# Performance work log

Hardware: AMD Instinct MI355X
Metric: run time of the kernel (lower is better)

The kernel has to match this reference:

```python
import jax, jax.numpy as jnp
import numpy as np

B, N = 2, 200
IMG = 2048
NC = 4                    # node concepts ('Is*')
NODE_CH = NC * 256        # 1024
EC = 3                    # edge concepts minus 'HigherPri'
AC = 4                    # actions
BBOX_MAX = 1024.0
E = N * (N - 1)

# static fully-connected directed edge list (src=i, dst=j, i!=j), row-major order
_ii, _jj = np.meshgrid(np.arange(N), np.arange(N), indexing='ij')
_m = _ii != _jj
SRC = jnp.asarray(_ii[_m])
DST = jnp.asarray(_jj[_m])


def _lin(k, fin, fout):
    kw, kb = jax.random.split(k)
    s = 1.0 / np.sqrt(fin)
    return (jax.random.uniform(kw, (fin, fout), jnp.float32, -s, s),
            jax.random.uniform(kb, (fout,), jnp.float32, -s, s))


def setup_inputs():
    ks = jax.random.split(jax.random.key(0), 16)
    p = {}
    p['roi_features'] = jax.random.normal(ks[0], (B, N, IMG), jnp.float32)
    p['batch_bboxes'] = jax.random.uniform(ks[1], (B, N, 4), jnp.float32) * BBOX_MAX
    p['batch_directions'] = jax.random.normal(ks[2], (B, N, 4), jnp.float32)
    p['batch_priorities'] = jax.random.normal(ks[3], (B, N), jnp.float32)
    p['w1'], p['b1'] = _lin(ks[4], IMG, 512)
    p['w2'], p['b2'] = _lin(ks[5], 512, 256)
    p['w3'], p['b3'] = _lin(ks[6], 256, NODE_CH)
    p['wi'], p['bi'] = _lin(ks[7], NODE_CH, NC)
    p['we1'], p['be1'] = _lin(ks[8], 16, 256)
    p['we2'], p['be2'] = _lin(ks[9], 256, 64)
    p['we3'], p['be3'] = _lin(ks[10], 64, EC)
    p['wp1'], p['bp1'] = _lin(ks[11], EC + 1, 128)
    p['wp2'], p['bp2'] = _lin(ks[12], 128, NODE_CH * AC)
    p['root_w'], _ = _lin(ks[13], NODE_CH, AC)
    _, p['root_b'] = _lin(ks[14], NODE_CH, AC)
    return p


def reference(roi_features, batch_bboxes, batch_directions, batch_priorities,
              w1, b1, w2, b2, w3, b3, wi, bi,
              we1, be1, we2, be2, we3, be3,
              wp1, bp1, wp2, bp2, root_w, root_b):
    # node concept embedding MLP: [B,N,IMG] -> [B,N,NODE_CH]
    h = jax.nn.relu(roi_features @ w1 + b1)
    h = jax.nn.relu(h @ w2 + b2)
    node_concepts = h @ w3 + b3
    node_concepts_explicit = jax.nn.sigmoid(node_concepts @ wi + bi)

    # pairwise attributes for all directed edges (same ordering as torch masks)
    node_attr = jnp.concatenate([batch_bboxes / BBOX_MAX, batch_directions], -1)  # [B,N,8]
    pair = jnp.concatenate([node_attr[:, SRC], node_attr[:, DST]], -1)            # [B,E,16]
    eh = jax.nn.relu(pair @ we1 + be1)
    eh = jax.nn.relu(eh @ we2 + be2)
    edge_attributes = jax.nn.sigmoid(eh @ we3 + be3)                              # [B,E,EC]
    higher_pri = (batch_priorities[:, SRC] > batch_priorities[:, DST]).astype(jnp.float32)
    edge_attributes = jnp.concatenate([edge_attributes, higher_pri[..., None]], -1)  # [B,E,EC+1]

    # NNConv on graph 0: per-edge weight matrix, gather-matmul-scatter
    x = node_concepts[0]                 # [N, NODE_CH]
    e = edge_attributes[0]               # [E, EC+1]
    w = jax.nn.relu(e @ wp1 + bp1) @ wp2 + bp2
    w = w.reshape(E, NODE_CH, AC)        # [E, NODE_CH, AC]
    msg = jnp.einsum('ei,eio->eo', x[SRC], w)          # [E, AC]
    agg = jax.ops.segment_sum(msg, DST, num_segments=N)  # [N, AC]
    next_actions = agg + x @ root_w + root_b
    return (next_actions, node_concepts_explicit[0], edge_attributes[0])
```

## Files before the change

### kernel.cpp

```cpp
#include <hip/hip_runtime.h>
#include <math.h>

#define NN 200
#define ETOT 39800

typedef float float4v __attribute__((ext_vector_type(4)));
typedef short short8 __attribute__((ext_vector_type(8)));
typedef unsigned int uint4v __attribute__((ext_vector_type(4)));

__device__ __forceinline__ float sigf(float x) { return 1.0f / (1.0f + expf(-x)); }

__device__ __forceinline__ unsigned short f2b(float f) {
  unsigned u = __float_as_uint(f);
  u += 0x7fffu + ((u >> 16) & 1u);
  return (unsigned short)(u >> 16);
}
__device__ __forceinline__ float b2f16(unsigned short u) {
  return __uint_as_float(((unsigned)u) << 16);
}
__device__ __forceinline__ unsigned pk2(float a, float b) {
  unsigned r;
  asm("v_cvt_pk_bf16_f32 %0, %1, %2" : "=v"(r) : "v"(a), "v"(b));
  return r;
}

__global__ __launch_bounds__(256) void k_prep(
    const float* __restrict__ w1, const float* __restrict__ w2, const float* __restrict__ w3,
    const float* __restrict__ b3, const float* __restrict__ wp2, const float* __restrict__ we2,
    const float* __restrict__ bbox, const float* __restrict__ dir,
    const float* __restrict__ we1, const float* __restrict__ be1,
    const float* __restrict__ roi, const float* __restrict__ wp1,
    const float* __restrict__ wi, const float* __restrict__ rootw, const float* __restrict__ bp2,
    unsigned short* __restrict__ w1T, unsigned short* __restrict__ w2T,
    unsigned short* __restrict__ Ac, unsigned short* __restrict__ Bc,
    unsigned short* __restrict__ we2T, unsigned short* __restrict__ roiB,
    float* __restrict__ P, float* __restrict__ Q, float* __restrict__ wp1T) {
  __shared__ float lds[64][65];
  const int b = blockIdx.x, tid = threadIdx.x;

  if (b < 288) {
    const float* Wf;
    unsigned short* Wt;
    int K, N, t;
    if (b < 256) { Wf = w1; Wt = w1T; K = 2048; N = 512; t = b; }
    else { Wf = w2; Wt = w2T; K = 512; N = 256; t = b - 256; }
    const int K64 = K >> 6;
    const int kt = t % K64, nt = t / K64;
#pragma unroll 4
    for (int i = 0; i < 16; ++i) {
      int idx = tid + i * 256;
      int r = idx >> 6, c = idx & 63;
      lds[r][c] = Wf[(size_t)(kt * 64 + r) * N + nt * 64 + c];
    }
    __syncthreads();
#pragma unroll 4
    for (int i = 0; i < 16; ++i) {
      int idx = tid + i * 256;
      int r = idx >> 6, c = idx & 63;
      Wt[(size_t)(nt * 64 + r) * K + kt * 64 + c] = f2b(lds[c][r]);
    }
  } else if (b < 416) {
    int k = b - 288;
    int o = tid >> 6, l = tid & 63;
    const float* src = wp2 + (size_t)k * 4096;
    unsigned short* dst = Ac + (size_t)(k * 4 + o) * 1024;
    for (int i = l; i < 1024; i += 64) dst[i] = f2b(src[i * 4 + o]);
  } else if (b < 432) {
    int r = b - 416;
    unsigned short* dst = Ac + (size_t)(512 + r) * 1024;
    const float* src = (r < 4) ? (wi + r) : (r < 8) ? (rootw + (r - 4))
                     : (r < 12) ? (bp2 + (r - 8)) : nullptr;
    for (int i = tid; i < 1024; i += 256)
      dst[i] = src ? f2b(src[i * 4]) : (unsigned short)0;
  } else if (b < 500) {
    int rb = (b - 432) * 4;
#pragma unroll
    for (int j = 0; j < 16; ++j) {
      int idx = tid + j * 256;
      int row = rb + (idx >> 10), i = idx & 1023;
      float val = (row < 256) ? w3[(size_t)row * 1024 + i] : (row == 256 ? b3[i] : 0.0f);
      Bc[(size_t)row * 1024 + i] = f2b(val);
    }
  } else if (b < 516) {
    int f = (b - 500) * 256 + tid;
    int c = f >> 6, k0 = (f & 63) * 4;
#pragma unroll
    for (int q = 0; q < 4; ++q)
      we2T[c * 256 + k0 + q] = f2b(we2[(k0 + q) * 64 + c]);
  } else if (b < 716) {
    int n = b - 516, c = tid;
    float a[8];
#pragma unroll
    for (int r = 0; r < 4; ++r) a[r] = bbox[n * 4 + r] * (1.0f / 1024.0f);
#pragma unroll
    for (int r = 0; r < 4; ++r) a[4 + r] = dir[n * 4 + r];
    float p = be1[c], q = 0.0f;
#pragma unroll
    for (int r = 0; r < 8; ++r) {
      p += a[r] * we1[r * 256 + c];
      q += a[r] * we1[(8 + r) * 256 + c];
    }
    P[n * 256 + c] = p;
    Q[n * 256 + c] = q;
  } else if (b < 916) {
    int n = b - 716;
    const float4v* R4 = (const float4v*)(roi + (size_t)n * 2048);
    unsigned long long* O = (unsigned long long*)(roiB + (size_t)n * 2048);
#pragma unroll
    for (int j = 0; j < 2; ++j) {
      int idx = tid + j * 256;
      float4v v = R4[idx];
      union { unsigned u[2]; unsigned long long ll; } pk;
      pk.u[0] = pk2(v[0], v[1]);
      pk.u[1] = pk2(v[2], v[3]);
      O[idx] = pk.ll;
    }
  } else {
    if (tid < 128) {
      float4v v = {wp1[tid], wp1[128 + tid], wp1[256 + tid], wp1[384 + tid]};
      ((float4v*)wp1T)[tid] = v;
    }
  }
}

__device__ __forceinline__ float4v mfma16(short8 a, short8 b, float4v c) {
  return __builtin_amdgcn_mfma_f32_16x16x32_bf16(a, b, c, 0, 0, 0);
}

template <int KSTEPS>
__device__ __forceinline__ float tile_core(const unsigned short* __restrict__ A,
                                           const unsigned short* __restrict__ B,
                                           int m0, int n0, int K,
                                           float (&red)[4][16][17]) {
  const int tid = threadIdx.x, lane = tid & 63, wv = tid >> 6;
  const int mr = lane & 15, quad = lane >> 4;
  const unsigned short* Ap = A + (size_t)(m0 + mr) * K + wv * (KSTEPS * 32) + quad * 8;
  const unsigned short* Bp = B + (size_t)(n0 + mr) * K + wv * (KSTEPS * 32) + quad * 8;
  float4v acc0 = {0.f, 0.f, 0.f, 0.f}, acc1 = {0.f, 0.f, 0.f, 0.f};
#pragma unroll
  for (int s = 0; s < KSTEPS; s += 2) {
    acc0 = mfma16(*(const short8*)(Ap + s * 32), *(const short8*)(Bp + s * 32), acc0);
    acc1 = mfma16(*(const short8*)(Ap + (s + 1) * 32), *(const short8*)(Bp + (s + 1) * 32), acc1);
  }
  float4v acc = acc0 + acc1;
#pragma unroll
  for (int r = 0; r < 4; ++r) red[wv][quad * 4 + r][mr] = acc[r];
  __syncthreads();
  const int row = tid >> 4, col = tid & 15;
  return red[0][row][col] + red[1][row][col] + red[2][row][col] + red[3][row][col];
}

__global__ __launch_bounds__(256) void k_gemm1_compose(
    const unsigned short* __restrict__ roiB, const unsigned short* __restrict__ w1T,
    const float* __restrict__ b1, unsigned short* __restrict__ h1,
    const unsigned short* __restrict__ Ac, const unsigned short* __restrict__ Bc,
    unsigned short* __restrict__ CT, float* __restrict__ biasT) {
  __shared__ float red[4][16][17];
  const int bid = blockIdx.x, tid = threadIdx.x;
  if (bid < 416) {
    const int m0 = (bid % 13) * 16, n0 = (bid / 13) * 16;
    float v = tile_core<16>(roiB, w1T, m0, n0, 2048, red);
    const int row = tid >> 4, col = tid & 15;
    v += b1[n0 + col];
    v = fmaxf(v, 0.f);
    h1[(size_t)(m0 + row) * 512 + n0 + col] = f2b(v);
  } else {
    const int t = bid - 416;
    const int m0 = (t % 33) * 16, n0 = (t / 33) * 16;
    float v = tile_core<8>(Ac, Bc, m0, n0, 1024, red);
    const int row = tid >> 4, col = tid & 15;
    const int c = n0 + col;
    if (c < 256) CT[(size_t)(m0 + row) * 256 + c] = f2b(v);
    else if (c == 256) biasT[m0 + row] = v;
  }
}

__global__ __launch_bounds__(256) void k_gemm2(const unsigned short* __restrict__ h1,
                                               const unsigned short* __restrict__ w2T,
                                               const float* __restrict__ b2,
                                               unsigned short* __restrict__ h2) {
  __shared__ float red[4][16][17];
  const int m0 = blockIdx.x * 16, n0 = blockIdx.y * 16, tid = threadIdx.x;
  float v = tile_core<4>(h1, w2T, m0, n0, 512, red);
  const int row = tid >> 4, col = tid & 15;
  v += b2[n0 + col];
  v = fmaxf(v, 0.f);
  h2[(size_t)(m0 + row) * 256 + n0 + col] = f2b(v);
}

__global__ __launch_bounds__(256) void k_tfused(const unsigned short* __restrict__ h2,
                                                const unsigned short* __restrict__ CT,
                                                const float* __restrict__ biasT,
                                                const float* __restrict__ bi,
                                                const float* __restrict__ rootb,
                                                float* __restrict__ Tm, float* __restrict__ out1,
                                                float* __restrict__ out0, float* __restrict__ U) {
  __shared__ float red[4][16][17];
  const int m0 = blockIdx.x * 16, n0 = blockIdx.y * 16, tid = threadIdx.x;
  float v = tile_core<2>(h2, CT, m0, n0, 256, red);
  const int row = tid >> 4, col = tid & 15;
  const int n = m0 + row, c = n0 + col;
  v += biasT[c];
  if (c < 512) {
    Tm[(size_t)n * 512 + c] = v;
  } else if (n < NN) {
    int r = c - 512;
    if (r < 4) out1[n * 4 + r] = sigf(v + bi[r]);
    else if (r < 8) out0[n * 4 + (r - 4)] = v + rootb[r - 4];
    else if (r < 12) U[n * 4 + (r - 8)] = v;
  }
}

__global__ __launch_bounds__(256) void k_edge(
    const float* __restrict__ P, const float* __restrict__ Q,
    const unsigned short* __restrict__ we2T,
    const float* __restrict__ be2, const float* __restrict__ we3, const float* __restrict__ be3,
    const float* __restrict__ wp1T, const float* __restrict__ bp1,
    const float* __restrict__ pri,
    const float* __restrict__ T, const float* __restrict__ U,
    float* __restrict__ out0, float* __restrict__ out_ea) {
  __shared__ int src_s[64], dst_s[64];
  __shared__ float ea_s[64][4];
  __shared__ float4v wp1s[128];
  __shared__ float bp1s[128];
  __shared__ float4v Ts[2][128];
  __shared__ float Us[2][4];

  const int tid = threadIdx.x;
  const int e0 = blockIdx.x * 64;
  const int s_lo = e0 / 199;

  if (tid < 64) {
    int e = e0 + tid;
    int i = -1, j = 0;
    if (e < ETOT) {
      i = e / 199;
      int jj = e - i * 199;
      j = jj + (jj >= i ? 1 : 0);
    }
    src_s[tid] = i;
    dst_s[tid] = j;
  }
  if (tid < 128) {
    wp1s[tid] = ((const float4v*)wp1T)[tid];
    bp1s[tid] = bp1[tid];
  }
  {
    int row = tid >> 7, c = tid & 127;
    Ts[row][c] = ((const float4v*)T)[(s_lo + row) * 128 + c];
  }
  if (tid < 8) {
    int s = min(s_lo + (tid >> 2), 199);
    Us[tid >> 2][tid & 3] = U[s * 4 + (tid & 3)];
  }
  __syncthreads();

  const int lane = tid & 63;
  const int wv = tid >> 6;
  const int m = lane & 15;
  const int quad = lane >> 4;
  const int eloc = wv * 16 + m;
  const int si = src_s[eloc];
  const int dj = dst_s[eloc];

  float4v acc[4];
#pragma unroll
  for (int ct = 0; ct < 4; ++ct) { acc[ct][0] = 0.f; acc[ct][1] = 0.f; acc[ct][2] = 0.f; acc[ct][3] = 0.f; }

  const short8* W8 = (const short8*)we2T;

  for (int ks = 0; ks < 8; ++ks) {
    union { short8 s; uint4v u; } af;
    af.s = (short8)0;
    if (si >= 0) {
      const float4v* p4 = (const float4v*)(P + si * 256 + ks * 32 + quad * 8);
      const float4v* q4 = (const float4v*)(Q + dj * 256 + ks * 32 + quad * 8);
      float4v v0 = p4[0] + q4[0];
      float4v v1 = p4[1] + q4[1];
      af.u[0] = pk2(fmaxf(v0[0], 0.f), fmaxf(v0[1], 0.f));
      af.u[1] = pk2(fmaxf(v0[2], 0.f), fmaxf(v0[3], 0.f));
      af.u[2] = pk2(fmaxf(v1[0], 0.f), fmaxf(v1[1], 0.f));
      af.u[3] = pk2(fmaxf(v1[2], 0.f), fmaxf(v1[3], 0.f));
    }
#pragma unroll
    for (int ct = 0; ct < 4; ++ct) {
      short8 bf = W8[(ct * 16 + m) * 32 + ks * 4 + quad];
      acc[ct] = __builtin_amdgcn_mfma_f32_16x16x32_bf16(af.s, bf, acc[ct], 0, 0, 0);
    }
  }

  float ev[4][3];
#pragma unroll
  for (int r = 0; r < 4; ++r) { ev[r][0] = 0.f; ev[r][1] = 0.f; ev[r][2] = 0.f; }
#pragma unroll
  for (int ct = 0; ct < 4; ++ct) {
    const int col = ct * 16 + m;
    const float b2v = be2[col];
    const float w0 = we3[col * 3 + 0], w1v = we3[col * 3 + 1], w2v = we3[col * 3 + 2];
#pragma unroll
    for (int r = 0; r < 4; ++r) {
      float e2 = fmaxf(acc[ct][r] + b2v, 0.f);
      ev[r][0] += e2 * w0;
      ev[r][1] += e2 * w1v;
      ev[r][2] += e2 * w2v;
    }
  }
#pragma unroll
  for (int r = 0; r < 4; ++r)
#pragma unroll
    for (int p = 0; p < 3; ++p) {
      float v = ev[r][p];
      v += __shfl_xor(v, 1, 64);
      v += __shfl_xor(v, 2, 64);
      v += __shfl_xor(v, 4, 64);
      v += __shfl_xor(v, 8, 64);
      ev[r][p] = v;
    }
  if (m == 0) {
#pragma unroll
    for (int r = 0; r < 4; ++r) {
      int el = wv * 16 + quad * 4 + r;
      int ss = src_s[el], dd = dst_s[el];
      if (ss >= 0) {
        float4v o;
        o[0] = sigf(ev[r][0] + be3[0]);
        o[1] = sigf(ev[r][1] + be3[1]);
        o[2] = sigf(ev[r][2] + be3[2]);
        o[3] = (pri[ss] > pri[dd]) ? 1.0f : 0.0f;
        *(float4v*)&ea_s[el][0] = o;
        *(float4v*)(out_ea + (size_t)(e0 + el) * 4) = o;
      }
    }
  }
  __syncthreads();

  const int ee = tid >> 2, pp = tid & 3;
  const int s2 = src_s[ee], d2 = dst_s[ee];
  float4v pm = {0.f, 0.f, 0.f, 0.f};
  if (s2 >= 0) {
    const int srow = s2 - s_lo;
    const float c0 = ea_s[ee][0], c1 = ea_s[ee][1], c2 = ea_s[ee][2], c3 = ea_s[ee][3];
#pragma unroll 8
    for (int t = pp; t < 128; t += 4) {
      float4v w4 = wp1s[t];
      float hv = bp1s[t] + c0 * w4[0] + c1 * w4[1] + c2 * w4[2] + c3 * w4[3];
      hv = fmaxf(hv, 0.f);
      pm += hv * Ts[srow][t];
    }
  }
#pragma unroll
  for (int o = 0; o < 4; ++o) {
    float v = pm[o];
    v += __shfl_xor(v, 1, 64);
    v += __shfl_xor(v, 2, 64);
    pm[o] = v;
  }
  if (s2 >= 0) atomicAdd(&out0[d2 * 4 + pp], Us[s2 - s_lo][pp] + pm[pp]);
}

extern "C" void kernel_launch(void* const* d_in, const int* in_sizes, int n_in,
                              void* d_out, int out_size, void* d_ws, size_t ws_size,
                              hipStream_t stream) {
  (void)in_sizes; (void)n_in; (void)out_size; (void)ws_size;
  const float* roi   = (const float*)d_in[0];
  const float* bbox  = (const float*)d_in[1];
  const float* dir   = (const float*)d_in[2];
  const float* pri   = (const float*)d_in[3];
  const float* w1    = (const float*)d_in[4];
  const float* b1    = (const float*)d_in[5];
  const float* w2    = (const float*)d_in[6];
  const float* b2    = (const float*)d_in[7];
  const float* w3    = (const float*)d_in[8];
  const float* b3    = (const float*)d_in[9];
  const float* wi    = (const float*)d_in[10];
  const float* bi    = (const float*)d_in[11];
  const float* we1   = (const float*)d_in[12];
  const float* be1   = (const float*)d_in[13];
  const float* we2   = (const float*)d_in[14];
  const float* be2   = (const float*)d_in[15];
  const float* we3   = (const float*)d_in[16];
  const float* be3   = (const float*)d_in[17];
  const float* wp1   = (const float*)d_in[18];
  const float* bp1   = (const float*)d_in[19];
  const float* wp2   = (const float*)d_in[20];
  const float* bp2   = (const float*)d_in[21];
  const float* rootw = (const float*)d_in[22];
  const float* rootb = (const float*)d_in[23];

  float* out0 = (float*)d_out;
  float* out1 = out0 + 800;
  float* out2 = out0 + 1600;

  unsigned short* us = (unsigned short*)d_ws;
  unsigned short* w1T  = us;
  unsigned short* w2T  = us + 1048576;
  unsigned short* Ac   = us + 1179648;
  unsigned short* Bc   = us + 1720320;
  unsigned short* we2T = us + 1998848;
  unsigned short* roiB = us + 2015232;
  unsigned short* h1   = us + 2441216;
  unsigned short* h2   = us + 2547712;
  unsigned short* CT   = us + 2600960;
  float* fb    = (float*)(us + 2736128);
  float* Tm    = fb;
  float* Pm    = fb + 106496;
  float* Qm    = fb + 157696;
  float* Um    = fb + 208896;
  float* wp1Tp = fb + 209696;
  float* biasT = fb + 210208;

  k_prep<<<917, 256, 0, stream>>>(w1, w2, w3, b3, wp2, we2, bbox, dir, we1, be1, roi, wp1,
                                  wi, rootw, bp2,
                                  w1T, w2T, Ac, Bc, we2T, roiB, Pm, Qm, wp1Tp);

  k_gemm1_compose<<<977, 256, 0, stream>>>(roiB, w1T, b1, h1, Ac, Bc, CT, biasT);

  k_gemm2<<<dim3(13, 16), 256, 0, stream>>>(h1, w2T, b2, h2);

  k_tfused<<<dim3(13, 33), 256, 0, stream>>>(h2, CT, biasT, bi, rootb, Tm, out1, out0, Um);

  k_edge<<<622, 256, 0, stream>>>(Pm, Qm, we2T, be2, we3, be3, wp1Tp, bp1, pri, Tm, Um, out0, out2);
}
```

Measured before the change: 154.4 us.

## Rebalance kernel stages: move weight prep into gemm1, compose into gemm2, halve edge blocks

The prep kernel now only transposes w1 and converts roi to bf16. The other weight conversions and the edge-MLP precompute move into the gemm1 kernel as extra blocks, and the Ac·Bc compose GEMM moves into the gemm2 kernel using a two-tile variant that reuses A fragments. The goal is a shorter critical path through the dependent launches, with independent work filling idle CUs. The edge kernel shrinks to 128 threads and 32 edges per block, doubling the grid. The Bc workspace offsets are shifted.

```diff
diff --git a/kernel.cpp b/kernel.cpp
--- a/kernel.cpp
+++ b/kernel.cpp
@@ -15,95 +15,90 @@
   u += 0x7fffu + ((u >> 16) & 1u);
   return (unsigned short)(u >> 16);
 }
-__device__ __forceinline__ float b2f16(unsigned short u) {
-  return __uint_as_float(((unsigned)u) << 16);
-}
 __device__ __forceinline__ unsigned pk2(float a, float b) {
   unsigned r;
   asm("v_cvt_pk_bf16_f32 %0, %1, %2" : "=v"(r) : "v"(a), "v"(b));
   return r;
 }
+__device__ __forceinline__ float4v mfma16(short8 a, short8 b, float4v c) {
+  return __builtin_amdgcn_mfma_f32_16x16x32_bf16(a, b, c, 0, 0, 0);
+}
+
+union SharedU {
+  float trans[64][65];
+  float red[4][16][34];
+};
+
+template <int KSTEPS>
+__device__ __forceinline__ float tile_core(const unsigned short* __restrict__ A,
+                                           const unsigned short* __restrict__ B,
+                                           int m0, int n0, int K, float (&red)[4][16][34]) {
+  const int tid = threadIdx.x, lane = tid & 63, wv = tid >> 6;
+  const int mr = lane & 15, quad = lane >> 4;
+  const unsigned short* Ap = A + (size_t)(m0 + mr) * K + wv * (KSTEPS * 32) + quad * 8;
+  const unsigned short* Bp = B + (size_t)(n0 + mr) * K + wv * (KSTEPS * 32) + quad * 8;
+  float4v acc0 = {0.f, 0.f, 0.f, 0.f}, acc1 = {0.f, 0.f, 0.f, 0.f};
+#pragma unroll
+  for (int s = 0; s < KSTEPS; s += 2) {
+    acc0 = mfma16(*(const short8*)(Ap + s * 32), *(const short8*)(Bp + s * 32), acc0);
+    acc1 = mfma16(*(const short8*)(Ap + (s + 1) * 32), *(const short8*)(Bp + (s + 1) * 32), acc1);
+  }
+  float4v acc = acc0 + acc1;
+#pragma unroll
+  for (int r = 0; r < 4; ++r) red[wv][quad * 4 + r][mr] = acc[r];
+  __syncthreads();
+  const int row = tid >> 4, col = tid & 15;
+  return red[0][row][col] + red[1][row][col] + red[2][row][col] + red[3][row][col];
+}
+
+template <int KSTEPS>
+__device__ __forceinline__ void tile_core2(const unsigned short* __restrict__ A,
+                                           const unsigned short* __restrict__ B,
+                                           int m0, int n0, int K,
+                                           float& v0, float& v1, float (&red)[4][16][34]) {
+  const int tid = threadIdx.x, lane = tid & 63, wv = tid >> 6;
+  const int mr = lane & 15, quad = lane >> 4;
+  const unsigned short* Ap = A + (size_t)(m0 + mr) * K + wv * (KSTEPS * 32) + quad * 8;
+  const unsigned short* B0 = B + (size_t)(n0 + mr) * K + wv * (KSTEPS * 32) + quad * 8;
+  const unsigned short* B1 = B0 + (size_t)16 * K;
+  float4v a0 = {0.f, 0.f, 0.f, 0.f}, a1 = {0.f, 0.f, 0.f, 0.f};
+#pragma unroll
+  for (int s = 0; s < KSTEPS; ++s) {
+    short8 af = *(const short8*)(Ap + s * 32);
+    a0 = mfma16(af, *(const short8*)(B0 + s * 32), a0);
+    a1 = mfma16(af, *(const short8*)(B1 + s * 32), a1);
+  }
+#pragma unroll
+  for (int r = 0; r < 4; ++r) {
+    red[wv][quad * 4 + r][mr] = a0[r];
+    red[wv][quad * 4 + r][17 + mr] = a1[r];
+  }
+  __syncthreads();
+  const int row = tid >> 4, col = tid & 15;
+  v0 = red[0][row][col] + red[1][row][col] + red[2][row][col] + red[3][row][col];
+  v1 = red[0][row][17 + col] + red[1][row][17 + col] + red[2][row][17 + col] + red[3][row][17 + col];
+}
 
 __global__ __launch_bounds__(256) void k_prep(
-    const float* __restrict__ w1, const float* __restrict__ w2, const float* __restrict__ w3,
-    const float* __restrict__ b3, const float* __restrict__ wp2, const float* __restrict__ we2,
-    const float* __restrict__ bbox, const float* __restrict__ dir,
-    const float* __restrict__ we1, const float* __restrict__ be1,
-    const float* __restrict__ roi, const float* __restrict__ wp1,
-    const float* __restrict__ wi, const float* __restrict__ rootw, const float* __restrict__ bp2,
-    unsigned short* __restrict__ w1T, unsigned short* __restrict__ w2T,
-    unsigned short* __restrict__ Ac, unsigned short* __restrict__ Bc,
-    unsigned short* __restrict__ we2T, unsigned short* __restrict__ roiB,
-    float* __restrict__ P, float* __restrict__ Q, float* __restrict__ wp1T) {
+    const float* __restrict__ w1, const float* __restrict__ roi,
+    unsigned short* __restrict__ w1T, unsigned short* __restrict__ roiB) {
   __shared__ float lds[64][65];
   const int b = blockIdx.x, tid = threadIdx.x;
-
-  if (b < 288) {
-    const float* Wf;
-    unsigned short* Wt;
-    int K, N, t;
-    if (b < 256) { Wf = w1; Wt = w1T; K = 2048; N = 512; t = b; }
-    else { Wf = w2; Wt = w2T; K = 512; N = 256; t = b - 256; }
-    const int K64 = K >> 6;
-    const int kt = t % K64, nt = t / K64;
+  if (b < 256) {
+    const int kt = b % 32, nt = b / 32;
 #pragma unroll 4
     for (int i = 0; i < 16; ++i) {
-      int idx = tid + i * 256;
-      int r = idx >> 6, c = idx & 63;
-      lds[r][c] = Wf[(size_t)(kt * 64 + r) * N + nt * 64 + c];
+      int idx = tid + i * 256, r = idx >> 6, c = idx & 63;
+      lds[r][c] = w1[(size_t)(kt * 64 + r) * 512 + nt * 64 + c];
     }
     __syncthreads();
 #pragma unroll 4
     for (int i = 0; i < 16; ++i) {
-      int idx = tid + i * 256;
-      int r = idx >> 6, c = idx & 63;
-      Wt[(size_t)(nt * 64 + r) * K + kt * 64 + c] = f2b(lds[c][r]);
-    }
-  } else if (b < 416) {
-    int k = b - 288;
-    int o = tid >> 6, l = tid & 63;
-    const float* src = wp2 + (size_t)k * 4096;
-    unsigned short* dst = Ac + (size_t)(k * 4 + o) * 1024;
-    for (int i = l; i < 1024; i += 64) dst[i] = f2b(src[i * 4 + o]);
-  } else if (b < 432) {
-    int r = b - 416;
-    unsigned short* dst = Ac + (size_t)(512 + r) * 1024;
-    const float* src = (r < 4) ? (wi + r) : (r < 8) ? (rootw + (r - 4))
-                     : (r < 12) ? (bp2 + (r - 8)) : nullptr;
-    for (int i = tid; i < 1024; i += 256)
-      dst[i] = src ? f2b(src[i * 4]) : (unsigned short)0;
-  } else if (b < 500) {
-    int rb = (b - 432) * 4;
-#pragma unroll
-    for (int j = 0; j < 16; ++j) {
-      int idx = tid + j * 256;
-      int row = rb + (idx >> 10), i = idx & 1023;
-      float val = (row < 256) ? w3[(size_t)row * 1024 + i] : (row == 256 ? b3[i] : 0.0f);
-      Bc[(size_t)row * 1024 + i] = f2b(val);
-    }
-  } else if (b < 516) {
-    int f = (b - 500) * 256 + tid;
-    int c = f >> 6, k0 = (f & 63) * 4;
-#pragma unroll
-    for (int q = 0; q < 4; ++q)
-      we2T[c * 256 + k0 + q] = f2b(we2[(k0 + q) * 64 + c]);
-  } else if (b < 716) {
-    int n = b - 516, c = tid;
-    float a[8];
-#pragma unroll
-    for (int r = 0; r < 4; ++r) a[r] = bbox[n * 4 + r] * (1.0f / 1024.0f);
-#pragma unroll
-    for (int r = 0; r < 4; ++r) a[4 + r] = dir[n * 4 + r];
-    float p = be1[c], q = 0.0f;
-#pragma unroll
-    for (int r = 0; r < 8; ++r) {
-      p += a[r] * we1[r * 256 + c];
-      q += a[r] * we1[(8 + r) * 256 + c];
-    }
-    P[n * 256 + c] = p;
-    Q[n * 256 + c] = q;
-  } else if (b < 916) {
-    int n = b - 716;
+      int idx = tid + i * 256, r = idx >> 6, c = idx & 63;
+      w1T[(size_t)(nt * 64 + r) * 2048 + kt * 64 + c] = f2b(lds[c][r]);
+    }
+  } else {
+    int n = b - 256;
     const float4v* R4 = (const float4v*)(roi + (size_t)n * 2048);
     unsigned long long* O = (unsigned long long*)(roiB + (size_t)n * 2048);
 #pragma unroll
@@ -115,6 +110,87 @@
       pk.u[1] = pk2(v[2], v[3]);
       O[idx] = pk.ll;
     }
+  }
+}
+
+__global__ __launch_bounds__(256) void k_g1x(
+    const unsigned short* __restrict__ roiB, const unsigned short* __restrict__ w1T,
+    const float* __restrict__ b1, unsigned short* __restrict__ h1,
+    const float* __restrict__ w2, unsigned short* __restrict__ w2T,
+    const float* __restrict__ wp2, const float* __restrict__ wi,
+    const float* __restrict__ rootw, const float* __restrict__ bp2,
+    unsigned short* __restrict__ Ac,
+    const float* __restrict__ w3, const float* __restrict__ b3, unsigned short* __restrict__ Bc,
+    const float* __restrict__ we2, unsigned short* __restrict__ we2T,
+    const float* __restrict__ bbox, const float* __restrict__ dir,
+    const float* __restrict__ we1, const float* __restrict__ be1,
+    float* __restrict__ P, float* __restrict__ Q,
+    const float* __restrict__ wp1, float* __restrict__ wp1T) {
+  __shared__ SharedU sh;
+  const int t = blockIdx.x, tid = threadIdx.x;
+  if (t < 416) {
+    const int m0 = (t % 13) * 16, n0 = (t / 13) * 16;
+    float v = tile_core<16>(roiB, w1T, m0, n0, 2048, sh.red);
+    const int row = tid >> 4, col = tid & 15;
+    v += b1[n0 + col];
+    v = fmaxf(v, 0.f);
+    h1[(size_t)(m0 + row) * 512 + n0 + col] = f2b(v);
+  } else if (t < 448) {
+    const int tt = t - 416, kt = tt % 8, nt = tt / 8;
+#pragma unroll 4
+    for (int i = 0; i < 16; ++i) {
+      int idx = tid + i * 256, r = idx >> 6, c = idx & 63;
+      sh.trans[r][c] = w2[(size_t)(kt * 64 + r) * 256 + nt * 64 + c];
+    }
+    __syncthreads();
+#pragma unroll 4
+    for (int i = 0; i < 16; ++i) {
+      int idx = tid + i * 256, r = idx >> 6, c = idx & 63;
+      w2T[(size_t)(nt * 64 + r) * 512 + kt * 64 + c] = f2b(sh.trans[c][r]);
+    }
+  } else if (t < 576) {
+    int k = t - 448;
+    int o = tid >> 6, l = tid & 63;
+    const float* src = wp2 + (size_t)k * 4096;
+    unsigned short* dst = Ac + (size_t)(k * 4 + o) * 1024;
+    for (int i = l; i < 1024; i += 64) dst[i] = f2b(src[i * 4 + o]);
+  } else if (t < 592) {
+    int r = t - 576;
+    unsigned short* dst = Ac + (size_t)(512 + r) * 1024;
+    const float* src = (r < 4) ? (wi + r) : (r < 8) ? (rootw + (r - 4))
+                     : (r < 12) ? (bp2 + (r - 8)) : nullptr;
+    for (int i = tid; i < 1024; i += 256)
+      dst[i] = src ? f2b(src[i * 4]) : (unsigned short)0;
+  } else if (t < 664) {
+    int rb = (t - 592) * 4;
+#pragma unroll
+    for (int j = 0; j < 16; ++j) {
+      int idx = tid + j * 256;
+      int row = rb + (idx >> 10), i = idx & 1023;
+      float val = (row < 256) ? w3[(size_t)row * 1024 + i] : (row == 256 ? b3[i] : 0.0f);
+      Bc[(size_t)row * 1024 + i] = f2b(val);
+    }
+  } else if (t < 680) {
+    int f = (t - 664) * 256 + tid;
+    int c = f >> 6, k0 = (f & 63) * 4;
+#pragma unroll
+    for (int q = 0; q < 4; ++q)
+      we2T[c * 256 + k0 + q] = f2b(we2[(k0 + q) * 64 + c]);
+  } else if (t < 880) {
+    int n = t - 680, c = tid;
+    float aa[8];
+#pragma unroll
+    for (int r = 0; r < 4; ++r) aa[r] = bbox[n * 4 + r] * (1.0f / 1024.0f);
+#pragma unroll
+    for (int r = 0; r < 4; ++r) aa[4 + r] = dir[n * 4 + r];
+    float p = be1[c], q = 0.0f;
+#pragma unroll
+    for (int r = 0; r < 8; ++r) {
+      p += aa[r] * we1[r * 256 + c];
+      q += aa[r] * we1[(8 + r) * 256 + c];
+    }
+    P[n * 256 + c] = p;
+    Q[n * 256 + c] = q;
   } else {
     if (tid < 128) {
       float4v v = {wp1[tid], wp1[128 + tid], wp1[256 + tid], wp1[384 + tid]};
@@ -123,69 +199,32 @@
   }
 }
 
-__device__ __forceinline__ float4v mfma16(short8 a, short8 b, float4v c) {
-  return __builtin_amdgcn_mfma_f32_16x16x32_bf16(a, b, c, 0, 0, 0);
-}
-
-template <int KSTEPS>
-__device__ __forceinline__ float tile_core(const unsigned short* __restrict__ A,
-                                           const unsigned short* __restrict__ B,
-                                           int m0, int n0, int K,
-                                           float (&red)[4][16][17]) {
-  const int tid = threadIdx.x, lane = tid & 63, wv = tid >> 6;
-  const int mr = lane & 15, quad = lane >> 4;
-  const unsigned short* Ap = A + (size_t)(m0 + mr) * K + wv * (KSTEPS * 32) + quad * 8;
-  const unsigned short* Bp = B + (size_t)(n0 + mr) * K + wv * (KSTEPS * 32) + quad * 8;
-  float4v acc0 = {0.f, 0.f, 0.f, 0.f}, acc1 = {0.f, 0.f, 0.f, 0.f};
-#pragma unroll
-  for (int s = 0; s < KSTEPS; s += 2) {
-    acc0 = mfma16(*(const short8*)(Ap + s * 32), *(const short8*)(Bp + s * 32), acc0);
-    acc1 = mfma16(*(const short8*)(Ap + (s + 1) * 32), *(const short8*)(Bp + (s + 1) * 32), acc1);
-  }
-  float4v acc = acc0 + acc1;
-#pragma unroll
-  for (int r = 0; r < 4; ++r) red[wv][quad * 4 + r][mr] = acc[r];
-  __syncthreads();
-  const int row = tid >> 4, col = tid & 15;
-  return red[0][row][col] + red[1][row][col] + red[2][row][col] + red[3][row][col];
-}
-
-__global__ __launch_bounds__(256) void k_gemm1_compose(
-    const unsigned short* __restrict__ roiB, const unsigned short* __restrict__ w1T,
-    const float* __restrict__ b1, unsigned short* __restrict__ h1,
+__global__ __launch_bounds__(256) void k_g2x(
+    const unsigned short* __restrict__ h1, const unsigned short* __restrict__ w2T,
+    const float* __restrict__ b2, unsigned short* __restrict__ h2,
     const unsigned short* __restrict__ Ac, const unsigned short* __restrict__ Bc,
     unsigned short* __restrict__ CT, float* __restrict__ biasT) {
-  __shared__ float red[4][16][17];
-  const int bid = blockIdx.x, tid = threadIdx.x;
-  if (bid < 416) {
-    const int m0 = (bid % 13) * 16, n0 = (bid / 13) * 16;
-    float v = tile_core<16>(roiB, w1T, m0, n0, 2048, red);
+  __shared__ SharedU sh;
+  const int t = blockIdx.x, tid = threadIdx.x;
+  if (t < 208) {
+    const int m0 = (t % 13) * 16, n0 = (t / 13) * 16;
+    float v = tile_core<4>(h1, w2T, m0, n0, 512, sh.red);
     const int row = tid >> 4, col = tid & 15;
-    v += b1[n0 + col];
+    v += b2[n0 + col];
     v = fmaxf(v, 0.f);
-    h1[(size_t)(m0 + row) * 512 + n0 + col] = f2b(v);
+    h2[(size_t)(m0 + row) * 256 + n0 + col] = f2b(v);
   } else {
-    const int t = bid - 416;
-    const int m0 = (t % 33) * 16, n0 = (t / 33) * 16;
-    float v = tile_core<8>(Ac, Bc, m0, n0, 1024, red);
+    const int u = t - 208, mi = u % 33, nj = u / 33;
+    const int m0 = mi * 16, n0 = nj * 32;
+    float v0, v1;
+    tile_core2<8>(Ac, Bc, m0, n0, 1024, v0, v1, sh.red);
     const int row = tid >> 4, col = tid & 15;
-    const int c = n0 + col;
-    if (c < 256) CT[(size_t)(m0 + row) * 256 + c] = f2b(v);
-    else if (c == 256) biasT[m0 + row] = v;
-  }
-}
-
-__global__ __launch_bounds__(256) void k_gemm2(const unsigned short* __restrict__ h1,
-                                               const unsigned short* __restrict__ w2T,
-                                               const float* __restrict__ b2,
-                                               unsigned short* __restrict__ h2) {
-  __shared__ float red[4][16][17];
-  const int m0 = blockIdx.x * 16, n0 = blockIdx.y * 16, tid = threadIdx.x;
-  float v = tile_core<4>(h1, w2T, m0, n0, 512, red);
-  const int row = tid >> 4, col = tid & 15;
-  v += b2[n0 + col];
-  v = fmaxf(v, 0.f);
-  h2[(size_t)(m0 + row) * 256 + n0 + col] = f2b(v);
+    const int m = m0 + row;
+    const int c0 = n0 + col, c1 = n0 + 16 + col;
+    if (c0 < 256) CT[(size_t)m * 256 + c0] = f2b(v0);
+    else if (c0 == 256) biasT[m] = v0;
+    if (c1 < 256) CT[(size_t)m * 256 + c1] = f2b(v1);
+  }
 }
 
 __global__ __launch_bounds__(256) void k_tfused(const unsigned short* __restrict__ h2,
@@ -195,9 +234,9 @@
                                                 const float* __restrict__ rootb,
                                                 float* __restrict__ Tm, float* __restrict__ out1,
                                                 float* __restrict__ out0, float* __restrict__ U) {
-  __shared__ float red[4][16][17];
+  __shared__ SharedU sh;
   const int m0 = blockIdx.x * 16, n0 = blockIdx.y * 16, tid = threadIdx.x;
-  float v = tile_core<2>(h2, CT, m0, n0, 256, red);
+  float v = tile_core<2>(h2, CT, m0, n0, 256, sh.red);
   const int row = tid >> 4, col = tid & 15;
   const int n = m0 + row, c = n0 + col;
   v += biasT[c];
@@ -211,7 +250,7 @@
   }
 }
 
-__global__ __launch_bounds__(256) void k_edge(
+__global__ __launch_bounds__(128) void k_edge(
     const float* __restrict__ P, const float* __restrict__ Q,
     const unsigned short* __restrict__ we2T,
     const float* __restrict__ be2, const float* __restrict__ we3, const float* __restrict__ be3,
@@ -219,18 +258,18 @@
     const float* __restrict__ pri,
     const float* __restrict__ T, const float* __restrict__ U,
     float* __restrict__ out0, float* __restrict__ out_ea) {
-  __shared__ int src_s[64], dst_s[64];
-  __shared__ float ea_s[64][4];
+  __shared__ int src_s[32], dst_s[32];
+  __shared__ float ea_s[32][4];
   __shared__ float4v wp1s[128];
   __shared__ float bp1s[128];
   __shared__ float4v Ts[2][128];
   __shared__ float Us[2][4];
 
   const int tid = threadIdx.x;
-  const int e0 = blockIdx.x * 64;
+  const int e0 = blockIdx.x * 32;
   const int s_lo = e0 / 199;
 
-  if (tid < 64) {
+  if (tid < 32) {
     int e = e0 + tid;
     int i = -1, j = 0;
     if (e < ETOT) {
@@ -241,12 +280,12 @@
     src_s[tid] = i;
     dst_s[tid] = j;
   }
-  if (tid < 128) {
-    wp1s[tid] = ((const float4v*)wp1T)[tid];
-    bp1s[tid] = bp1[tid];
-  }
-  {
-    int row = tid >> 7, c = tid & 127;
+  wp1s[tid] = ((const float4v*)wp1T)[tid];
+  bp1s[tid] = bp1[tid];
+#pragma unroll
+  for (int j = 0; j < 2; ++j) {
+    int idx = tid + j * 128;
+    int row = idx >> 7, c = idx & 127;
     Ts[row][c] = ((const float4v*)T)[(s_lo + row) * 128 + c];
   }
   if (tid < 8) {
@@ -341,11 +380,11 @@
     const int srow = s2 - s_lo;
     const float c0 = ea_s[ee][0], c1 = ea_s[ee][1], c2 = ea_s[ee][2], c3 = ea_s[ee][3];
 #pragma unroll 8
-    for (int t = pp; t < 128; t += 4) {
-      float4v w4 = wp1s[t];
-      float hv = bp1s[t] + c0 * w4[0] + c1 * w4[1] + c2 * w4[2] + c3 * w4[3];
+    for (int tt = pp; tt < 128; tt += 4) {
+      float4v w4 = wp1s[tt];
+      float hv = bp1s[tt] + c0 * w4[0] + c1 * w4[1] + c2 * w4[2] + c3 * w4[3];
       hv = fmaxf(hv, 0.f);
-      pm += hv * Ts[srow][t];
+      pm += hv * Ts[srow][tt];
     }
   }
 #pragma unroll
@@ -396,12 +435,12 @@
   unsigned short* w2T  = us + 1048576;
   unsigned short* Ac   = us + 1179648;
   unsigned short* Bc   = us + 1720320;
-  unsigned short* we2T = us + 1998848;
-  unsigned short* roiB = us + 2015232;
-  unsigned short* h1   = us + 2441216;
-  unsigned short* h2   = us + 2547712;
-  unsigned short* CT   = us + 2600960;
-  float* fb    = (float*)(us + 2736128);
+  unsigned short* we2T = us + 2015232;
+  unsigned short* roiB = us + 2031616;
+  unsigned short* h1   = us + 2457600;
+  unsigned short* h2   = us + 2564096;
+  unsigned short* CT   = us + 2617344;
+  float* fb    = (float*)(us + 2752512);
   float* Tm    = fb;
   float* Pm    = fb + 106496;
   float* Qm    = fb + 157696;
@@ -409,15 +448,19 @@
   float* wp1Tp = fb + 209696;
   float* biasT = fb + 210208;
 
-  k_prep<<<917, 256, 0, stream>>>(w1, w2, w3, b3, wp2, we2, bbox, dir, we1, be1, roi, wp1,
-                                  wi, rootw, bp2,
-                                  w1T, w2T, Ac, Bc, we2T, roiB, Pm, Qm, wp1Tp);
-
-  k_gemm1_compose<<<977, 256, 0, stream>>>(roiB, w1T, b1, h1, Ac, Bc, CT, biasT);
-
-  k_gemm2<<<dim3(13, 16), 256, 0, stream>>>(h1, w2T, b2, h2);
+  k_prep<<<456, 256, 0, stream>>>(w1, roi, w1T, roiB);
+
+  k_g1x<<<881, 256, 0, stream>>>(roiB, w1T, b1, h1,
+                                 w2, w2T,
+                                 wp2, wi, rootw, bp2, Ac,
+                                 w3, b3, Bc,
+                                 we2, we2T,
+                                 bbox, dir, we1, be1, Pm, Qm,
+                                 wp1, wp1Tp);
+
+  k_g2x<<<505, 256, 0, stream>>>(h1, w2T, b2, h2, Ac, Bc, CT, biasT);
 
   k_tfused<<<dim3(13, 33), 256, 0, stream>>>(h2, CT, biasT, bi, rootb, Tm, out1, out0, Um);
 
-  k_edge<<<622, 256, 0, stream>>>(Pm, Qm, we2T, be2, we3, be3, wp1Tp, bp1, pri, Tm, Um, out0, out2);
-}
+  k_edge<<<1244, 128, 0, stream>>>(Pm, Qm, we2T, be2, we3, be3, wp1Tp, bp1, pri, Tm, Um, out0, out2);
+}
```

Result: no change. 157.0 us (+1.7%).
